# Kernel tuning notes

Measured on AMD Instinct MI355X. Metric: run time of the kernel, lower is better.

Reference implementation:

```python
import jax, jax.numpy as jnp
import numpy as np

B, S, H, NH = 4, 2048, 1024, 16
D = H // NH  # d_per_head = 64


def setup_inputs() -> dict:
    key = jax.random.key(0)
    ks = jax.random.split(key, 6)
    return {
        "x": jax.random.normal(ks[0], (B, S, H), dtype=jnp.float32),
        "W_query": jax.random.uniform(ks[1], (NH, D, H), dtype=jnp.float32),
        "W_key": jax.random.uniform(ks[2], (NH, D, H), dtype=jnp.float32),
        "W_value": jax.random.uniform(ks[3], (NH, D, H), dtype=jnp.float32),
        "W_out": jax.random.normal(ks[4], (H, H), dtype=jnp.float32) * 0.02,
        "b_out": jnp.zeros((H,), dtype=jnp.float32),
    }


def reference(x, W_query, W_key, W_value, W_out, b_out):
    b, s, h = x.shape
    n_head, d, _ = W_query.shape
    # ALiBi: slope_i = -(i+1); distance[q, k] = k - q (non-causal, full softmax)
    dist = (jnp.arange(s)[None, :] - jnp.arange(s)[:, None]).astype(x.dtype)  # [s, s]
    slopes = -(jnp.arange(1, n_head + 1, dtype=x.dtype))  # [n_head]
    # per-head projections: x @ W[i].T  -> [b, n, s, d]
    q = jnp.einsum("bsh,ndh->bnsd", x, W_query)
    k = jnp.einsum("bsh,ndh->bnsd", x, W_key)
    v = jnp.einsum("bsh,ndh->bnsd", x, W_value)
    scores = jnp.einsum("bnqd,bnkd->bnqk", q, k) / jnp.sqrt(jnp.asarray(d, x.dtype))
    scores = scores + slopes[None, :, None, None] * dist[None, None, :, :]
    attn = jax.nn.softmax(scores, axis=-1)
    heads = jnp.einsum("bnqk,bnkd->bnqd", attn, v)  # [b, n, s, d]
    # concat heads along feature dim (head 0 first, matching torch cat order)
    multi = heads.transpose(0, 2, 1, 3).reshape(b, s, n_head * d)
    return multi @ W_out.T + b_out
```

## Files before the change

kernel.cpp:

```cpp
#include <hip/hip_runtime.h>
#include <hip/hip_bf16.h>
#include <stdint.h>

typedef unsigned short u16;
typedef short bf16x8 __attribute__((ext_vector_type(8)));
typedef float f32x4 __attribute__((ext_vector_type(4)));

#define DEV __device__ __forceinline__

DEV u16 f2bf(float f) {
  union { float f; uint32_t u; } v; v.f = f;
  uint32_t u = v.u;
  return (u16)((u + 0x7FFFu + ((u >> 16) & 1u)) >> 16);
}
DEV u16 f2bf_fast(float f) {
  union { float f; uint32_t u; } v; v.f = f;
  return (u16)((v.u + 0x8000u) >> 16);
}
DEV float bf2f(u16 h) {
  union { uint32_t u; float f; } v; v.u = ((uint32_t)h) << 16;
  return v.f;
}
DEV uint32_t cvtpk_bf16(float lo, float hi) {
  uint32_t r;
  asm volatile("v_cvt_pk_bf16_f32 %0, %1, %2" : "=v"(r) : "v"(lo), "v"(hi));
  return r;
}

#if __has_builtin(__builtin_amdgcn_exp2f)
#define EXP2F(x) __builtin_amdgcn_exp2f(x)
#else
#define EXP2F(x) exp2f(x)
#endif

#define GLL(gp, lp) __builtin_amdgcn_global_load_lds(\
    (const __attribute__((address_space(1))) unsigned int*)(gp), \
    (__attribute__((address_space(3))) unsigned int*)(lp), 16, 0, 0)

__global__ void prep_x(const float* __restrict__ x, u16* __restrict__ xh, u16* __restrict__ xl) {
  int i = blockIdx.x * 256 + threadIdx.x;
  float4 v = ((const float4*)x)[i];
  ushort4 h, lo;
  h.x = f2bf(v.x); h.y = f2bf(v.y); h.z = f2bf(v.z); h.w = f2bf(v.w);
  lo.x = f2bf(v.x - bf2f(h.x)); lo.y = f2bf(v.y - bf2f(h.y));
  lo.z = f2bf(v.z - bf2f(h.z)); lo.w = f2bf(v.w - bf2f(h.w));
  ((ushort4*)xh)[i] = h;
  ((ushort4*)xl)[i] = lo;
}

__global__ void prep_w(const float* __restrict__ wq, const float* __restrict__ wk,
                       const float* __restrict__ wv, const float* __restrict__ wo,
                       u16* __restrict__ wqkh, u16* __restrict__ wqkl,
                       u16* __restrict__ wvb, u16* __restrict__ wob) {
  int i = blockIdx.x * 256 + threadIdx.x;
  int seg = i >> 18;
  int j = i & ((1 << 18) - 1);
  const float* src = (seg == 0) ? wq : (seg == 1) ? wk : (seg == 2) ? wv : wo;
  float4 v = ((const float4*)src)[j];
  ushort4 h;
  h.x = f2bf(v.x); h.y = f2bf(v.y); h.z = f2bf(v.z); h.w = f2bf(v.w);
  if (seg < 2) {
    ushort4 lo;
    lo.x = f2bf(v.x - bf2f(h.x)); lo.y = f2bf(v.y - bf2f(h.y));
    lo.z = f2bf(v.z - bf2f(h.z)); lo.w = f2bf(v.w - bf2f(h.w));
    ((ushort4*)wqkh)[i] = h;
    ((ushort4*)wqkl)[i] = lo;
  } else if (seg == 2) {
    ((ushort4*)wvb)[j] = h;
  } else {
    ((ushort4*)wob)[j] = h;
  }
}

__global__ __launch_bounds__(256, 2) void qkv_gemm(
    const u16* __restrict__ xh, const u16* __restrict__ xl,
    const u16* __restrict__ wh, const u16* __restrict__ wl,
    const u16* __restrict__ wv,
    u16* __restrict__ qkh, u16* __restrict__ qkl, u16* __restrict__ vout) {
  __shared__ u16 Ah[128 * 32], Al[128 * 32], Bh[128 * 32], Bl[128 * 32];
  const int t = threadIdx.x, w = t >> 6, l = t & 63, g = l >> 4, lr = l & 15;
  const int m0 = blockIdx.y * 128, n0 = blockIdx.x * 128;
  const bool split = (n0 < 2048);
  const u16* bsrc_h = split ? (wh + (size_t)n0 * 1024) : (wv + (size_t)(n0 - 2048) * 1024);
  const u16* bsrc_l = split ? (wl + (size_t)n0 * 1024) : wl;
  const int wr = w >> 1, wc = w & 1;

  f32x4 zero = {0.f, 0.f, 0.f, 0.f};
  f32x4 acc[4][4];
#pragma unroll
  for (int mi = 0; mi < 4; ++mi)
#pragma unroll
    for (int ni = 0; ni < 4; ++ni) acc[mi][ni] = zero;

  for (int k0 = 0; k0 < 1024; k0 += 32) {
    __syncthreads();
#pragma unroll
    for (int i = 0; i < 2; ++i) {
      const int c = i * 256 + t;
      const int row = c >> 2;
      const int kc8 = (c & 3) * 8;
      const size_t goff = (size_t)row * 1024 + k0 + kc8;
      const int lo = i * 4096 + w * 1024;
      GLL(xh + (size_t)m0 * 1024 + goff, (char*)Ah + lo);
      GLL(bsrc_h + goff, (char*)Bh + lo);
      if (split) {
        GLL(xl + (size_t)m0 * 1024 + goff, (char*)Al + lo);
        GLL(bsrc_l + goff, (char*)Bl + lo);
      }
    }
    __syncthreads();

    bf16x8 ah[4], al[4];
#pragma unroll
    for (int mi = 0; mi < 4; ++mi) {
      const int idx = (wr * 64 + mi * 16 + lr) * 32 + g * 8;
      ah[mi] = *(const bf16x8*)&Ah[idx];
      if (split) al[mi] = *(const bf16x8*)&Al[idx];
    }
#pragma unroll
    for (int ni = 0; ni < 4; ++ni) {
      const int idx = (wc * 64 + ni * 16 + lr) * 32 + g * 8;
      bf16x8 bh = *(const bf16x8*)&Bh[idx];
      bf16x8 bl;
      if (split) bl = *(const bf16x8*)&Bl[idx];
#pragma unroll
      for (int mi = 0; mi < 4; ++mi) {
        acc[mi][ni] = __builtin_amdgcn_mfma_f32_16x16x32_bf16(ah[mi], bh, acc[mi][ni], 0, 0, 0);
        if (split) {
          acc[mi][ni] = __builtin_amdgcn_mfma_f32_16x16x32_bf16(al[mi], bh, acc[mi][ni], 0, 0, 0);
          acc[mi][ni] = __builtin_amdgcn_mfma_f32_16x16x32_bf16(ah[mi], bl, acc[mi][ni], 0, 0, 0);
        }
      }
    }
  }

#pragma unroll
  for (int mi = 0; mi < 4; ++mi)
#pragma unroll
    for (int ni = 0; ni < 4; ++ni)
#pragma unroll
      for (int r = 0; r < 4; ++r) {
        const int row = m0 + wr * 64 + mi * 16 + g * 4 + r;
        const int col = wc * 64 + ni * 16 + lr;
        const float cval = acc[mi][ni][r];
        if (split) {
          const u16 h = f2bf(cval);
          qkh[(size_t)row * 2048 + n0 + col] = h;
          qkl[(size_t)row * 2048 + n0 + col] = f2bf(cval - bf2f(h));
        } else {
          vout[(size_t)row * 1024 + (n0 - 2048) + col] = f2bf(cval);
        }
      }
}

__global__ __launch_bounds__(256) void vtrans(const u16* __restrict__ vin, u16* __restrict__ vout) {
  __shared__ u16 Ts[64 * 66];
  const int t = threadIdx.x;
  const int r0 = blockIdx.y * 64, c0 = blockIdx.x * 64;
  const int rl = t >> 3, cc = (t & 7) * 8;
#pragma unroll
  for (int i = 0; i < 2; ++i) {
    const int r = rl + i * 32;
    bf16x8 v = *(const bf16x8*)&vin[(size_t)(r0 + r) * 1024 + c0 + cc];
#pragma unroll
    for (int e = 0; e < 8; ++e) Ts[(cc + e) * 66 + r] = (u16)v[e];
  }
  __syncthreads();
  const int c = t >> 2, seg = (t & 3) * 16;
  u16 tmp[16];
#pragma unroll
  for (int e = 0; e < 16; ++e) tmp[e] = Ts[c * 66 + seg + e];
  *(bf16x8*)&vout[(size_t)(c0 + c) * 8192 + r0 + seg] = *(const bf16x8*)&tmp[0];
  *(bf16x8*)&vout[(size_t)(c0 + c) * 8192 + r0 + seg + 8] = *(const bf16x8*)&tmp[8];
}

__global__ __launch_bounds__(512, 2) void attn(
    const u16* __restrict__ qkh, const u16* __restrict__ qkl,
    const u16* __restrict__ vt, u16* __restrict__ multi) {
  __shared__ u16 Ksh[2][4096], Ksl[2][4096], Vts[2][4096];
  __shared__ u16 Ps[8][2048];
  const int t = threadIdx.x, w = t >> 6, l = t & 63, g = l >> 4, lr = l & 15;
  const int L = blockIdx.x;
  const int flat = (L & 7) * 64 + (L >> 3);
  const int b = flat >> 7, h = (flat >> 3) & 15, qt = flat & 7;
  const int q0 = qt * 256;
  const size_t rowbase = (size_t)b * 2048;
  const u16* Qh = qkh + rowbase * 2048 + h * 64;
  const u16* Ql = qkl + rowbase * 2048 + h * 64;
  const u16* Kh = qkh + rowbase * 2048 + 1024 + h * 64;
  const u16* Kl = qkl + rowbase * 2048 + 1024 + h * 64;
  const u16* Vb = vt + (size_t)(h * 64) * 8192 + b * 2048;

  const int srow = l >> 3;
  const int sj = (l & 7) ^ srow;
  const int krow = w * 8 + srow;
  const int ldsoff = w * 1024;
  u16* Pw = &Ps[w][0];

  bf16x8 qfh[2][2], qfl[2][2];
#pragma unroll
  for (int nt = 0; nt < 2; ++nt)
#pragma unroll
    for (int kc = 0; kc < 2; ++kc) {
      const size_t off = (size_t)(q0 + w * 32 + nt * 16 + lr) * 2048 + kc * 32 + g * 8;
      qfh[nt][kc] = *(const bf16x8*)&Qh[off];
      qfl[nt][kc] = *(const bf16x8*)&Ql[off];
    }

  f32x4 zero = {0.f, 0.f, 0.f, 0.f};
  f32x4 o[2][4];
#pragma unroll
  for (int mi = 0; mi < 2; ++mi)
#pragma unroll
    for (int dn = 0; dn < 4; ++dn) o[mi][dn] = zero;
  float mst[2] = {-3.0e38f, -3.0e38f};
  float lst[2] = {0.f, 0.f};

  const float c1 = 0.125f * 1.44269504088896f;
  const float slope2 = -(float)(h + 1) * 1.44269504088896f;
  const float s2r1 = slope2, s2r2 = slope2 * 2.0f, s2r3 = slope2 * 3.0f;
  float base[4];
#pragma unroll
  for (int mt = 0; mt < 4; ++mt) base[mt] = slope2 * (float)(mt * 16 + g * 4);
  const float bstep = slope2 * 64.0f;
  const int sbase = (l & 48) | (g * 4);

  GLL(Kh + (size_t)krow * 2048 + sj * 8, (char*)&Ksh[0][0] + ldsoff);
  GLL(Kl + (size_t)krow * 2048 + sj * 8, (char*)&Ksl[0][0] + ldsoff);
  GLL(Vb + (size_t)krow * 8192 + sj * 8, (char*)&Vts[0][0] + ldsoff);
  __syncthreads();

  int cur = 0;
  for (int kt = 0; kt < 2048; kt += 64) {
    if (kt + 64 < 2048) {
      const int nxt = cur ^ 1;
      GLL(Kh + (size_t)(kt + 64 + krow) * 2048 + sj * 8, (char*)&Ksh[nxt][0] + ldsoff);
      GLL(Kl + (size_t)(kt + 64 + krow) * 2048 + sj * 8, (char*)&Ksl[nxt][0] + ldsoff);
      GLL(Vb + (size_t)krow * 8192 + kt + 64 + sj * 8, (char*)&Vts[nxt][0] + ldsoff);
    }
    const u16* Kcur = &Ksh[cur][0];
    const u16* Lcur = &Ksl[cur][0];
    const u16* Vcur = &Vts[cur][0];

    f32x4 c[4][2];
#pragma unroll
    for (int mt = 0; mt < 4; ++mt)
#pragma unroll
      for (int nt = 0; nt < 2; ++nt) c[mt][nt] = zero;
    __builtin_amdgcn_s_setprio(1);
#pragma unroll
    for (int mt = 0; mt < 4; ++mt) {
      bf16x8 ah[2], al[2];
#pragma unroll
      for (int kc = 0; kc < 2; ++kc) {
        const int rk = mt * 16 + lr;
        const int byte = rk * 128 + (((kc * 4 + g) ^ (rk & 7)) << 4);
        ah[kc] = *(const bf16x8*)((const char*)Kcur + byte);
        al[kc] = *(const bf16x8*)((const char*)Lcur + byte);
      }
#pragma unroll
      for (int nt = 0; nt < 2; ++nt) {
        f32x4 a = c[mt][nt];
        a = __builtin_amdgcn_mfma_f32_16x16x32_bf16(ah[0], qfh[nt][0], a, 0, 0, 0);
        a = __builtin_amdgcn_mfma_f32_16x16x32_bf16(ah[1], qfh[nt][1], a, 0, 0, 0);
        a = __builtin_amdgcn_mfma_f32_16x16x32_bf16(al[0], qfh[nt][0], a, 0, 0, 0);
        a = __builtin_amdgcn_mfma_f32_16x16x32_bf16(al[1], qfh[nt][1], a, 0, 0, 0);
        a = __builtin_amdgcn_mfma_f32_16x16x32_bf16(ah[0], qfl[nt][0], a, 0, 0, 0);
        a = __builtin_amdgcn_mfma_f32_16x16x32_bf16(ah[1], qfl[nt][1], a, 0, 0, 0);
        c[mt][nt] = a;
      }
    }
    __builtin_amdgcn_s_setprio(0);

#pragma unroll
    for (int mt = 0; mt < 4; ++mt)
#pragma unroll
      for (int nt = 0; nt < 2; ++nt) {
        f32x4 a = c[mt][nt];
        a[0] = fmaf(a[0], c1, base[mt]);
        a[1] = fmaf(a[1], c1, base[mt] + s2r1);
        a[2] = fmaf(a[2], c1, base[mt] + s2r2);
        a[3] = fmaf(a[3], c1, base[mt] + s2r3);
        c[mt][nt] = a;
      }
    float rmax[2];
#pragma unroll
    for (int nt = 0; nt < 2; ++nt) {
      float m01 = fmaxf(fmaxf(c[0][nt][0], c[0][nt][1]), fmaxf(c[0][nt][2], c[0][nt][3]));
      float m23 = fmaxf(fmaxf(c[1][nt][0], c[1][nt][1]), fmaxf(c[1][nt][2], c[1][nt][3]));
      float m45 = fmaxf(fmaxf(c[2][nt][0], c[2][nt][1]), fmaxf(c[2][nt][2], c[2][nt][3]));
      float m67 = fmaxf(fmaxf(c[3][nt][0], c[3][nt][1]), fmaxf(c[3][nt][2], c[3][nt][3]));
      float m = fmaxf(fmaxf(m01, m23), fmaxf(m45, m67));
      m = fmaxf(m, __shfl_xor(m, 16));
      m = fmaxf(m, __shfl_xor(m, 32));
      rmax[nt] = m;
    }
    const bool need = (rmax[0] > mst[0]) | (rmax[1] > mst[1]);
    if (__any(need)) {
      float alpha_sm[2];
#pragma unroll
      for (int nt = 0; nt < 2; ++nt) {
        const float mn = fmaxf(mst[nt], rmax[nt]);
        alpha_sm[nt] = EXP2F(mst[nt] - mn);
        mst[nt] = mn;
        lst[nt] *= alpha_sm[nt];
      }
#pragma unroll
      for (int mi = 0; mi < 2; ++mi)
#pragma unroll
        for (int r = 0; r < 4; ++r) {
          const float al_o = __shfl(alpha_sm[mi], sbase + r);
#pragma unroll
          for (int dn = 0; dn < 4; ++dn) o[mi][dn][r] *= al_o;
        }
    }
#pragma unroll
    for (int nt = 0; nt < 2; ++nt) {
      const int q = nt * 16 + lr;
      const int rowb = q * 128;
      const int qs = (q & 7);
      float rsum = 0.f;
#pragma unroll
      for (int mt = 0; mt < 4; ++mt) {
        const float p0 = EXP2F(c[mt][nt][0] - mst[nt]);
        const float p1 = EXP2F(c[mt][nt][1] - mst[nt]);
        const float p2 = EXP2F(c[mt][nt][2] - mst[nt]);
        const float p3 = EXP2F(c[mt][nt][3] - mst[nt]);
        rsum += (p0 + p1) + (p2 + p3);
        uint2 pk;
        pk.x = cvtpk_bf16(p0, p1);
        pk.y = cvtpk_bf16(p2, p3);
        const int c16 = 2 * mt + (g >> 1);
        const int byte = rowb + ((c16 ^ qs) << 4) + (g & 1) * 8;
        *(uint2*)((char*)Pw + byte) = pk;
      }
      rsum += __shfl_xor(rsum, 16);
      rsum += __shfl_xor(rsum, 32);
      lst[nt] += rsum;
    }

    bf16x8 pa[2][2];
#pragma unroll
    for (int mi = 0; mi < 2; ++mi)
#pragma unroll
      for (int kc = 0; kc < 2; ++kc) {
        const int row = mi * 16 + lr;
        const int jk = kc * 4 + g;
        const int byte = row * 128 + ((jk ^ (row & 7)) << 4);
        pa[mi][kc] = *(const bf16x8*)((const char*)Pw + byte);
      }
    __builtin_amdgcn_s_setprio(1);
#pragma unroll
    for (int dn = 0; dn < 4; ++dn) {
      bf16x8 vb[2];
#pragma unroll
      for (int kc = 0; kc < 2; ++kc) {
        const int row = dn * 16 + lr;
        const int jk = kc * 4 + g;
        const int byte = row * 128 + ((jk ^ (row & 7)) << 4);
        vb[kc] = *(const bf16x8*)((const char*)Vcur + byte);
      }
#pragma unroll
      for (int mi = 0; mi < 2; ++mi) {
        o[mi][dn] = __builtin_amdgcn_mfma_f32_16x16x32_bf16(pa[mi][0], vb[0], o[mi][dn], 0, 0, 0);
        o[mi][dn] = __builtin_amdgcn_mfma_f32_16x16x32_bf16(pa[mi][1], vb[1], o[mi][dn], 0, 0, 0);
      }
    }
    __builtin_amdgcn_s_setprio(0);

#pragma unroll
    for (int mt = 0; mt < 4; ++mt) base[mt] += bstep;

    __syncthreads();
    cur ^= 1;
  }

#pragma unroll
  for (int mi = 0; mi < 2; ++mi)
#pragma unroll
    for (int r = 0; r < 4; ++r) {
      const float l_o = __shfl(lst[mi], sbase + r);
      const float rinv = 1.0f / l_o;
      const int qrow = q0 + w * 32 + mi * 16 + g * 4 + r;
#pragma unroll
      for (int dn = 0; dn < 4; ++dn) {
        const int d = dn * 16 + lr;
        multi[(rowbase + qrow) * 1024 + h * 64 + d] = f2bf_fast(o[mi][dn][r] * rinv);
      }
    }
}

__global__ __launch_bounds__(256, 2) void out_gemm(
    const u16* __restrict__ A, const u16* __restrict__ Bw,
    const float* __restrict__ bias, float* __restrict__ out) {
  __shared__ u16 As[128 * 32], Bs[128 * 32];
  const int t = threadIdx.x, w = t >> 6, l = t & 63, g = l >> 4, lr = l & 15;
  const int m0 = blockIdx.y * 128, n0 = blockIdx.x * 128;
  const int wr = w >> 1, wc = w & 1;

  f32x4 zero = {0.f, 0.f, 0.f, 0.f};
  f32x4 acc[4][4];
#pragma unroll
  for (int mi = 0; mi < 4; ++mi)
#pragma unroll
    for (int ni = 0; ni < 4; ++ni) acc[mi][ni] = zero;

  for (int k0 = 0; k0 < 1024; k0 += 32) {
    __syncthreads();
#pragma unroll
    for (int i = 0; i < 2; ++i) {
      const int c = i * 256 + t;
      const int row = c >> 2;
      const int kc8 = (c & 3) * 8;
      const size_t goff = (size_t)row * 1024 + k0 + kc8;
      const int lo = i * 4096 + w * 1024;
      GLL(A + (size_t)m0 * 1024 + goff, (char*)As + lo);
      GLL(Bw + (size_t)n0 * 1024 + goff, (char*)Bs + lo);
    }
    __syncthreads();

    bf16x8 ah[4];
#pragma unroll
    for (int mi = 0; mi < 4; ++mi)
      ah[mi] = *(const bf16x8*)&As[(wr * 64 + mi * 16 + lr) * 32 + g * 8];
#pragma unroll
    for (int ni = 0; ni < 4; ++ni) {
      bf16x8 bh = *(const bf16x8*)&Bs[(wc * 64 + ni * 16 + lr) * 32 + g * 8];
#pragma unroll
      for (int mi = 0; mi < 4; ++mi)
        acc[mi][ni] = __builtin_amdgcn_mfma_f32_16x16x32_bf16(ah[mi], bh, acc[mi][ni], 0, 0, 0);
    }
  }

#pragma unroll
  for (int mi = 0; mi < 4; ++mi)
#pragma unroll
    for (int ni = 0; ni < 4; ++ni)
#pragma unroll
      for (int r = 0; r < 4; ++r) {
        const int row = m0 + wr * 64 + mi * 16 + g * 4 + r;
        const int col = n0 + wc * 64 + ni * 16 + lr;
        out[(size_t)row * 1024 + col] = acc[mi][ni][r] + bias[col];
      }
}

extern "C" void kernel_launch(void* const* d_in, const int* in_sizes, int n_in,
                              void* d_out, int out_size, void* d_ws, size_t ws_size,
                              hipStream_t stream) {
  (void)in_sizes; (void)n_in; (void)out_size; (void)ws_size;
  const float* x  = (const float*)d_in[0];
  const float* wq = (const float*)d_in[1];
  const float* wk = (const float*)d_in[2];
  const float* wv = (const float*)d_in[3];
  const float* wo = (const float*)d_in[4];
  const float* bo = (const float*)d_in[5];
  float* out = (float*)d_out;
  char* ws = (char*)d_ws;

  const size_t MB = 1024 * 1024;
  u16* xh   = (u16*)(ws + 0);
  u16* xl   = (u16*)(ws + 16 * MB);
  u16* qkh  = (u16*)(ws + 32 * MB);
  u16* qkl  = (u16*)(ws + 64 * MB);
  u16* vbf  = (u16*)(ws + 96 * MB);
  u16* wqkh = (u16*)(ws + 112 * MB);
  u16* wqkl = (u16*)(ws + 116 * MB);
  u16* wvb  = (u16*)(ws + 120 * MB);
  u16* wob  = (u16*)(ws + 122 * MB);
  u16* multi = xh;
  u16* vt    = xl;

  prep_x<<<8192, 256, 0, stream>>>(x, xh, xl);
  prep_w<<<4096, 256, 0, stream>>>(wq, wk, wv, wo, wqkh, wqkl, wvb, wob);
  qkv_gemm<<<dim3(24, 64), 256, 0, stream>>>(xh, xl, wqkh, wqkl, wvb, qkh, qkl, vbf);
  vtrans<<<dim3(16, 128), 256, 0, stream>>>(vbf, vt);
  attn<<<512, 512, 0, stream>>>(qkh, qkl, vt, multi);
  out_gemm<<<dim3(8, 64), 256, 0, stream>>>(multi, wob, bo, out);
}
```

Before: 353.6 us.

## Keep P in registers by permuting K rows and transposing the PV MFMA

```diff
diff --git a/kernel.cpp b/kernel.cpp
--- a/kernel.cpp
+++ b/kernel.cpp
@@ -5,6 +5,7 @@
 typedef unsigned short u16;
 typedef short bf16x8 __attribute__((ext_vector_type(8)));
 typedef float f32x4 __attribute__((ext_vector_type(4)));
+typedef uint32_t u32x4 __attribute__((ext_vector_type(4)));
 
 #define DEV __device__ __forceinline__
 
@@ -12,10 +13,6 @@
   union { float f; uint32_t u; } v; v.f = f;
   uint32_t u = v.u;
   return (u16)((u + 0x7FFFu + ((u >> 16) & 1u)) >> 16);
-}
-DEV u16 f2bf_fast(float f) {
-  union { float f; uint32_t u; } v; v.f = f;
-  return (u16)((v.u + 0x8000u) >> 16);
 }
 DEV float bf2f(u16 h) {
   union { uint32_t u; float f; } v; v.u = ((uint32_t)h) << 16;
@@ -178,7 +175,6 @@
     const u16* __restrict__ qkh, const u16* __restrict__ qkl,
     const u16* __restrict__ vt, u16* __restrict__ multi) {
   __shared__ u16 Ksh[2][4096], Ksl[2][4096], Vts[2][4096];
-  __shared__ u16 Ps[8][2048];
   const int t = threadIdx.x, w = t >> 6, l = t & 63, g = l >> 4, lr = l & 15;
   const int L = blockIdx.x;
   const int flat = (L & 7) * 64 + (L >> 3);
@@ -194,8 +190,9 @@
   const int srow = l >> 3;
   const int sj = (l & 7) ^ srow;
   const int krow = w * 8 + srow;
+  const int klog = ((krow >> 5) << 5) | (((krow >> 2) & 3) << 3)
+                 | (((krow >> 4) & 1) << 2) | (krow & 3);
   const int ldsoff = w * 1024;
-  u16* Pw = &Ps[w][0];
 
   bf16x8 qfh[2][2], qfl[2][2];
 #pragma unroll
@@ -210,9 +207,9 @@
   f32x4 zero = {0.f, 0.f, 0.f, 0.f};
   f32x4 o[2][4];
 #pragma unroll
-  for (int mi = 0; mi < 2; ++mi)
-#pragma unroll
-    for (int dn = 0; dn < 4; ++dn) o[mi][dn] = zero;
+  for (int nt = 0; nt < 2; ++nt)
+#pragma unroll
+    for (int dn = 0; dn < 4; ++dn) o[nt][dn] = zero;
   float mst[2] = {-3.0e38f, -3.0e38f};
   float lst[2] = {0.f, 0.f};
 
@@ -221,12 +218,12 @@
   const float s2r1 = slope2, s2r2 = slope2 * 2.0f, s2r3 = slope2 * 3.0f;
   float base[4];
 #pragma unroll
-  for (int mt = 0; mt < 4; ++mt) base[mt] = slope2 * (float)(mt * 16 + g * 4);
+  for (int mt = 0; mt < 4; ++mt)
+    base[mt] = slope2 * (float)(((mt >> 1) << 5) + ((mt & 1) << 2) + g * 8);
   const float bstep = slope2 * 64.0f;
-  const int sbase = (l & 48) | (g * 4);
-
-  GLL(Kh + (size_t)krow * 2048 + sj * 8, (char*)&Ksh[0][0] + ldsoff);
-  GLL(Kl + (size_t)krow * 2048 + sj * 8, (char*)&Ksl[0][0] + ldsoff);
+
+  GLL(Kh + (size_t)klog * 2048 + sj * 8, (char*)&Ksh[0][0] + ldsoff);
+  GLL(Kl + (size_t)klog * 2048 + sj * 8, (char*)&Ksl[0][0] + ldsoff);
   GLL(Vb + (size_t)krow * 8192 + sj * 8, (char*)&Vts[0][0] + ldsoff);
   __syncthreads();
 
@@ -234,8 +231,8 @@
   for (int kt = 0; kt < 2048; kt += 64) {
     if (kt + 64 < 2048) {
       const int nxt = cur ^ 1;
-      GLL(Kh + (size_t)(kt + 64 + krow) * 2048 + sj * 8, (char*)&Ksh[nxt][0] + ldsoff);
-      GLL(Kl + (size_t)(kt + 64 + krow) * 2048 + sj * 8, (char*)&Ksl[nxt][0] + ldsoff);
+      GLL(Kh + (size_t)(kt + 64 + klog) * 2048 + sj * 8, (char*)&Ksh[nxt][0] + ldsoff);
+      GLL(Kl + (size_t)(kt + 64 + klog) * 2048 + sj * 8, (char*)&Ksl[nxt][0] + ldsoff);
       GLL(Vb + (size_t)krow * 8192 + kt + 64 + sj * 8, (char*)&Vts[nxt][0] + ldsoff);
     }
     const u16* Kcur = &Ksh[cur][0];
@@ -297,29 +294,24 @@
     }
     const bool need = (rmax[0] > mst[0]) | (rmax[1] > mst[1]);
     if (__any(need)) {
-      float alpha_sm[2];
 #pragma unroll
       for (int nt = 0; nt < 2; ++nt) {
         const float mn = fmaxf(mst[nt], rmax[nt]);
-        alpha_sm[nt] = EXP2F(mst[nt] - mn);
+        const float alpha = EXP2F(mst[nt] - mn);
         mst[nt] = mn;
-        lst[nt] *= alpha_sm[nt];
-      }
-#pragma unroll
-      for (int mi = 0; mi < 2; ++mi)
-#pragma unroll
-        for (int r = 0; r < 4; ++r) {
-          const float al_o = __shfl(alpha_sm[mi], sbase + r);
-#pragma unroll
-          for (int dn = 0; dn < 4; ++dn) o[mi][dn][r] *= al_o;
+        lst[nt] *= alpha;
+#pragma unroll
+        for (int dn = 0; dn < 4; ++dn) {
+          o[nt][dn][0] *= alpha; o[nt][dn][1] *= alpha;
+          o[nt][dn][2] *= alpha; o[nt][dn][3] *= alpha;
         }
-    }
+      }
+    }
+    bf16x8 pb[2][2];
 #pragma unroll
     for (int nt = 0; nt < 2; ++nt) {
-      const int q = nt * 16 + lr;
-      const int rowb = q * 128;
-      const int qs = (q & 7);
       float rsum = 0.f;
+      uint32_t pk01[4], pk23[4];
 #pragma unroll
       for (int mt = 0; mt < 4; ++mt) {
         const float p0 = EXP2F(c[mt][nt][0] - mst[nt]);
@@ -327,28 +319,19 @@
         const float p2 = EXP2F(c[mt][nt][2] - mst[nt]);
         const float p3 = EXP2F(c[mt][nt][3] - mst[nt]);
         rsum += (p0 + p1) + (p2 + p3);
-        uint2 pk;
-        pk.x = cvtpk_bf16(p0, p1);
-        pk.y = cvtpk_bf16(p2, p3);
-        const int c16 = 2 * mt + (g >> 1);
-        const int byte = rowb + ((c16 ^ qs) << 4) + (g & 1) * 8;
-        *(uint2*)((char*)Pw + byte) = pk;
+        pk01[mt] = cvtpk_bf16(p0, p1);
+        pk23[mt] = cvtpk_bf16(p2, p3);
       }
       rsum += __shfl_xor(rsum, 16);
       rsum += __shfl_xor(rsum, 32);
       lst[nt] += rsum;
-    }
-
-    bf16x8 pa[2][2];
-#pragma unroll
-    for (int mi = 0; mi < 2; ++mi)
-#pragma unroll
-      for (int kc = 0; kc < 2; ++kc) {
-        const int row = mi * 16 + lr;
-        const int jk = kc * 4 + g;
-        const int byte = row * 128 + ((jk ^ (row & 7)) << 4);
-        pa[mi][kc] = *(const bf16x8*)((const char*)Pw + byte);
-      }
+      union { u32x4 u; bf16x8 bf; } cv0, cv1;
+      cv0.u = (u32x4){pk01[0], pk23[0], pk01[1], pk23[1]};
+      cv1.u = (u32x4){pk01[2], pk23[2], pk01[3], pk23[3]};
+      pb[nt][0] = cv0.bf;
+      pb[nt][1] = cv1.bf;
+    }
+
     __builtin_amdgcn_s_setprio(1);
 #pragma unroll
     for (int dn = 0; dn < 4; ++dn) {
@@ -361,9 +344,9 @@
         vb[kc] = *(const bf16x8*)((const char*)Vcur + byte);
       }
 #pragma unroll
-      for (int mi = 0; mi < 2; ++mi) {
-        o[mi][dn] = __builtin_amdgcn_mfma_f32_16x16x32_bf16(pa[mi][0], vb[0], o[mi][dn], 0, 0, 0);
-        o[mi][dn] = __builtin_amdgcn_mfma_f32_16x16x32_bf16(pa[mi][1], vb[1], o[mi][dn], 0, 0, 0);
+      for (int nt = 0; nt < 2; ++nt) {
+        o[nt][dn] = __builtin_amdgcn_mfma_f32_16x16x32_bf16(vb[0], pb[nt][0], o[nt][dn], 0, 0, 0);
+        o[nt][dn] = __builtin_amdgcn_mfma_f32_16x16x32_bf16(vb[1], pb[nt][1], o[nt][dn], 0, 0, 0);
       }
     }
     __builtin_amdgcn_s_setprio(0);
@@ -376,18 +359,17 @@
   }
 
 #pragma unroll
-  for (int mi = 0; mi < 2; ++mi)
-#pragma unroll
-    for (int r = 0; r < 4; ++r) {
-      const float l_o = __shfl(lst[mi], sbase + r);
-      const float rinv = 1.0f / l_o;
-      const int qrow = q0 + w * 32 + mi * 16 + g * 4 + r;
-#pragma unroll
-      for (int dn = 0; dn < 4; ++dn) {
-        const int d = dn * 16 + lr;
-        multi[(rowbase + qrow) * 1024 + h * 64 + d] = f2bf_fast(o[mi][dn][r] * rinv);
-      }
-    }
+  for (int nt = 0; nt < 2; ++nt) {
+    const float rinv = 1.0f / lst[nt];
+    const int qrow = q0 + w * 32 + nt * 16 + lr;
+#pragma unroll
+    for (int dn = 0; dn < 4; ++dn) {
+      uint2 pkv;
+      pkv.x = cvtpk_bf16(o[nt][dn][0] * rinv, o[nt][dn][1] * rinv);
+      pkv.y = cvtpk_bf16(o[nt][dn][2] * rinv, o[nt][dn][3] * rinv);
+      *(uint2*)&multi[(rowbase + qrow) * 1024 + h * 64 + dn * 16 + g * 4] = pkv;
+    }
+  }
 }
 
 __global__ __launch_bounds__(256, 2) void out_gemm(
```

Result: no change. 347.5 us (-1.7%).
